# Kernel tuning notes

Hardware: AMD Instinct MI355X
Metric: run time of the kernel (lower is better)

Reference implementation:

```python
import jax, jax.numpy as jnp
import numpy as np

H3, W3, D3 = 12, 12, 12
NUM_HEADS = 8
DIM = 128
BATCH = 4
N_TOK = H3 * W3 * D3  # 1728
TABLE = (2 * H3 - 1) * (2 * W3 - 1) * (2 * D3 - 1)  # 12167


def _relative_position_index(h, w, d):
    ch, cw, cd = np.arange(h), np.arange(w), np.arange(d)
    coords = np.stack(np.meshgrid(ch, cw, cd, indexing='ij'))  # (3,h,w,d)
    cf = coords.reshape(3, -1)  # (3,N)
    rel = cf[:, :, None] - cf[:, None, :]  # (3,N,N)
    rel = rel.transpose(1, 2, 0).copy()
    rel[:, :, 0] += h - 1
    rel[:, :, 1] += w - 1
    rel[:, :, 2] += d - 1
    rel[:, :, 0] *= (2 * w - 1) * (2 * d - 1)
    rel[:, :, 1] *= 2 * d - 1
    return rel.sum(-1).astype(np.int32)  # (N,N)


def setup_inputs() -> dict:
    key = jax.random.key(0)
    ks = jax.random.split(key, 7)
    s = 1.0 / np.sqrt(DIM)
    return {
        'x': jax.random.normal(ks[0], (BATCH, N_TOK, DIM), jnp.float32),
        'Wq': jax.random.normal(ks[1], (DIM, DIM), jnp.float32) * s,
        'Wk': jax.random.normal(ks[2], (DIM, DIM), jnp.float32) * s,
        'Wv': jax.random.normal(ks[3], (DIM, DIM), jnp.float32) * s,
        'Wp': jax.random.normal(ks[4], (DIM, DIM), jnp.float32) * s,
        'bp': jnp.zeros((DIM,), jnp.float32),
        'rel_pos_table': jax.random.normal(ks[5], (TABLE, NUM_HEADS), jnp.float32) * 0.02,
        'rel_index': jnp.asarray(_relative_position_index(H3, W3, D3)),
    }


def reference(x, Wq, Wk, Wv, Wp, bp, rel_pos_table, rel_index):
    B, N, C = x.shape
    H = NUM_HEADS
    hd = C // H
    # projections (qkv_bias=False), split heads -> (B,H,N,hd)
    q = (x @ Wq.T).reshape(B, N, H, hd).transpose(0, 2, 1, 3)
    k = (x @ Wk.T).reshape(B, N, H, hd).transpose(0, 2, 1, 3)
    v = (x @ Wv.T).reshape(B, N, H, hd).transpose(0, 2, 1, 3)
    q_sig = jax.nn.sigmoid(q)
    # relative position bias: (N,N,H) -> (H,N,N)
    bias = rel_pos_table[rel_index.reshape(-1)].reshape(N, N, H).transpose(2, 0, 1)
    # softmax over key dim j of (k[b,h,j,d] + bias[h,i,j]) is separable:
    #   exp(k_jd + b_ij) = exp(b_ij - bmax_i) * exp(k_jd - kmax_d) * const
    kmax = jnp.max(k, axis=2, keepdims=True)            # (B,H,1,hd)
    bmax = jnp.max(bias, axis=2, keepdims=True)         # (H,N,1)
    ek = jnp.exp(k - kmax)                              # (B,H,N,hd)
    eb = jnp.exp(bias - bmax)                           # (H,N,N)
    num = jnp.einsum('hij,bhjd->bhid', eb, ek * v)      # (B,H,N,hd)
    den = jnp.einsum('hij,bhjd->bhid', eb, ek)          # (B,H,N,hd)
    out = q_sig * (num / den)                           # (B,H,N,hd)
    out = out.transpose(0, 2, 1, 3).reshape(B, N, C)
    return out @ Wp.T + bp
```

## Files before the change

### kernel.cpp

```cpp
#include <hip/hip_runtime.h>
#include <hip/hip_bf16.h>
#include <cmath>

#define NTOK 1728
#define DIMC 128
#define NHEAD 8
#define NB 4
#define TABN 12167
#define TSTRIDE 12168

typedef __attribute__((ext_vector_type(8))) short bf16x8;
typedef __attribute__((ext_vector_type(4))) float f32x4;

static __device__ __forceinline__ unsigned short f2bf(float f) {
    union { float f; unsigned u; } v; v.f = f;
    unsigned r = v.u + 0x7fff + ((v.u >> 16) & 1);
    return (unsigned short)(r >> 16);
}

static __device__ __forceinline__ int Pdec(int t) {
    return (t / 144) * 529 + ((t / 12) % 12) * 23 + (t % 12);
}

__global__ __launch_bounds__(256) void k_proj_qkv(
    const float* __restrict__ x, const float* __restrict__ Wq,
    const float* __restrict__ Wk, const float* __restrict__ Wv,
    const float* __restrict__ tbl, unsigned short* __restrict__ tblT,
    float* __restrict__ n1,
    float* __restrict__ QS, float* __restrict__ Ko, float* __restrict__ Vo)
{
    __shared__ __align__(16) float xs[64 * 128];
    __shared__ __align__(16) float Ws[32 * 128];
    const int t = threadIdx.x;
    const int m = blockIdx.z;
    if (m == 3) {
        const int bid2 = blockIdx.y * 108 + blockIdx.x;
        if (bid2 < 48) {
            const int idx = bid2 * 256 + t;
            if (idx < TABN) {
                float4 f0 = *reinterpret_cast<const float4*>(&tbl[idx * 8]);
                float4 f1 = *reinterpret_cast<const float4*>(&tbl[idx * 8 + 4]);
                tblT[0 * TSTRIDE + idx] = f2bf(expm1f(f0.x));
                tblT[1 * TSTRIDE + idx] = f2bf(expm1f(f0.y));
                tblT[2 * TSTRIDE + idx] = f2bf(expm1f(f0.z));
                tblT[3 * TSTRIDE + idx] = f2bf(expm1f(f0.w));
                tblT[4 * TSTRIDE + idx] = f2bf(expm1f(f1.x));
                tblT[5 * TSTRIDE + idx] = f2bf(expm1f(f1.y));
                tblT[6 * TSTRIDE + idx] = f2bf(expm1f(f1.z));
                tblT[7 * TSTRIDE + idx] = f2bf(expm1f(f1.w));
            }
        } else if (bid2 == 48) {
            ((float4*)n1)[t] = (float4){0.f, 0.f, 0.f, 0.f};
        }
        return;
    }
    const int row0 = blockIdx.x * 64;
    const int cg = blockIdx.y;
    const float* __restrict__ W = (m == 0) ? Wq : (m == 1) ? Wk : Wv;

    {
        const int cc = t & 31;
        #pragma unroll
        for (int p = 0; p < 8; ++p) {
            const int r = (t >> 5) + p * 8;
            float4 v = *reinterpret_cast<const float4*>(&x[(size_t)(row0 + r) * DIMC + cc * 4]);
            *reinterpret_cast<float4*>(&xs[r * 128 + ((cc * 4) ^ ((r & 7) << 2))]) = v;
        }
    }
    {
        const int cc = t & 31;
        #pragma unroll
        for (int p = 0; p < 4; ++p) {
            const int c = (t >> 5) + p * 8;
            float4 v = *reinterpret_cast<const float4*>(&W[(size_t)(cg * 32 + c) * DIMC + cc * 4]);
            *reinterpret_cast<float4*>(&Ws[c * 128 + cc * 4]) = v;
        }
    }
    __syncthreads();
    const int nl = t & 63, w = t >> 6;
    float acc[8];
    #pragma unroll
    for (int c = 0; c < 8; ++c) acc[c] = 0.f;
    for (int k4 = 0; k4 < 32; ++k4) {
        const float4 xv = *reinterpret_cast<const float4*>(
            &xs[nl * 128 + ((k4 * 4) ^ ((nl & 7) << 2))]);
        #pragma unroll
        for (int c = 0; c < 8; ++c) {
            const float4 wv = *reinterpret_cast<const float4*>(&Ws[(w * 8 + c) * 128 + k4 * 4]);
            acc[c] = fmaf(xv.x, wv.x, fmaf(xv.y, wv.y,
                     fmaf(xv.z, wv.z, fmaf(xv.w, wv.w, acc[c]))));
        }
    }
    if (m == 0) {
        #pragma unroll
        for (int c = 0; c < 8; ++c) acc[c] = 1.f / (1.f + expf(-acc[c]));
    }
    __syncthreads();
    float* res = Ws;
    #pragma unroll
    for (int c = 0; c < 8; ++c) res[nl * 33 + w * 8 + c] = acc[c];
    __syncthreads();
    float* __restrict__ Out = (m == 0) ? QS : (m == 1) ? Ko : Vo;
    {
        const int r = t >> 2, q = t & 3;
        float4 v0, v1;
        v0.x = res[r*33 + q*8 + 0]; v0.y = res[r*33 + q*8 + 1];
        v0.z = res[r*33 + q*8 + 2]; v0.w = res[r*33 + q*8 + 3];
        v1.x = res[r*33 + q*8 + 4]; v1.y = res[r*33 + q*8 + 5];
        v1.z = res[r*33 + q*8 + 6]; v1.w = res[r*33 + q*8 + 7];
        *reinterpret_cast<float4*>(&Out[(size_t)(row0 + r) * DIMC + cg * 32 + q * 8]) = v0;
        *reinterpret_cast<float4*>(&Out[(size_t)(row0 + r) * DIMC + cg * 32 + q * 8 + 4]) = v1;
    }
}

__global__ __launch_bounds__(256) void k_build_ekv(
    const float* __restrict__ Ko, const float* __restrict__ Vo,
    unsigned short* __restrict__ EKVt, float* __restrict__ n1)
{
    __shared__ float red[256][33];
    const int t = threadIdx.x;
    const int h = blockIdx.y;
    const int b = t >> 6, jj = t & 63;
    const int j = blockIdx.x * 64 + jj;
    const float* kp = &Ko[((size_t)b * NTOK + j) * DIMC + h * 16];
    const float* vp = &Vo[((size_t)b * NTOK + j) * DIMC + h * 16];
    float kv[16], vv[16], ob[32];
    #pragma unroll
    for (int d4 = 0; d4 < 4; ++d4) {
        *reinterpret_cast<float4*>(&kv[d4 * 4]) = *reinterpret_cast<const float4*>(&kp[d4 * 4]);
        *reinterpret_cast<float4*>(&vv[d4 * 4]) = *reinterpret_cast<const float4*>(&vp[d4 * 4]);
    }
    #pragma unroll
    for (int d = 0; d < 16; ++d) {
        float e = expf(kv[d]);
        ob[d] = e * vv[d];
        ob[16 + d] = e;
    }
    #pragma unroll
    for (int c = 0; c < 32; ++c)
        EKVt[((size_t)h * DIMC + b * 32 + c) * NTOK + j] = f2bf(ob[c]);
    #pragma unroll
    for (int c = 0; c < 32; ++c) red[t][c] = ob[c];
    __syncthreads();
    if (t < 128) {
        const int b2 = t >> 5, c = t & 31;
        float s = 0.f;
        for (int r = 0; r < 64; ++r) s += red[b2 * 64 + r][c];
        atomicAdd(&n1[(h * NB + b2) * 32 + c], s);
    }
}

__global__ __launch_bounds__(256) void k_aft_mfma(
    const unsigned short* __restrict__ tblT,
    const unsigned short* __restrict__ EKVt,
    float* __restrict__ part)
{
    __shared__ __align__(16) unsigned short slds[2304];
    __shared__ __align__(16) unsigned short alds[64 * 64];
    __shared__ __align__(16) unsigned short blds[128 * 64];
    const int t = threadIdx.x;
    const int i0 = blockIdx.x * 64;
    const int h = blockIdx.y;
    const int js = blockIdx.z;
    const int l = t & 63, w = t >> 6;
    const int il = l & 15, kg = l >> 4;

    const int j_base = js * 576;
    const int pj_lo = js * 4 * 529;
    const int pj_hi = pj_lo + 1851;
    const int idx_lo = Pdec(i0) + 6083 - pj_hi;
    {
        const unsigned short* src = &tblT[(size_t)h * TSTRIDE + idx_lo];
        #pragma unroll
        for (int p = 0; p < 9; ++p) slds[p * 256 + t] = src[p * 256 + t];
    }

    const int gi0 = w * 16;
    int qb[16];
    #pragma unroll
    for (int r = 0; r < 16; ++r) qb[r] = Pdec(i0 + gi0 + r) + 6083 - idx_lo;

    const int bc = t >> 3;
    const int bj8 = (t & 7) * 8;

    f32x4 acc[8];
    #pragma unroll
    for (int cf = 0; cf < 8; ++cf) acc[cf] = (f32x4){0.f, 0.f, 0.f, 0.f};

    for (int jt = 0; jt < 9; ++jt) {
        const int j0 = j_base + jt * 64;
        const int pj = Pdec(j0 + l);
        __syncthreads();
        #pragma unroll
        for (int p = 0; p < 4; ++p) {
            const int c = bc + p * 32;
            bf16x8 v = *reinterpret_cast<const bf16x8*>(
                &EKVt[((size_t)h * DIMC + c) * NTOK + j0 + bj8]);
            *reinterpret_cast<bf16x8*>(&blds[c * 64 + (bj8 ^ ((c & 7) << 3))]) = v;
        }
        #pragma unroll
        for (int r = 0; r < 16; ++r) {
            alds[(gi0 + r) * 64 + (l ^ ((r & 7) << 3))] = slds[qb[r] - pj];
        }
        __syncthreads();
        #pragma unroll
        for (int kk = 0; kk < 2; ++kk) {
            const int ia = w * 16 + il;
            const int ka = kk * 32 + kg * 8;
            bf16x8 af = *reinterpret_cast<const bf16x8*>(
                &alds[ia * 64 + (ka ^ ((ia & 7) << 3))]);
            #pragma unroll
            for (int cf = 0; cf < 8; ++cf) {
                const int cb = cf * 16 + il;
                bf16x8 bf = *reinterpret_cast<const bf16x8*>(
                    &blds[cb * 64 + (ka ^ ((cb & 7) << 3))]);
                acc[cf] = __builtin_amdgcn_mfma_f32_16x16x32_bf16(af, bf, acc[cf], 0, 0, 0);
            }
        }
    }
    #pragma unroll
    for (int cf = 0; cf < 8; ++cf) {
        #pragma unroll
        for (int r = 0; r < 4; ++r) {
            const int i = i0 + w * 16 + kg * 4 + r;
            const int c = cf * 16 + il;
            part[(((size_t)h * NTOK + i) * 3 + js) * DIMC + c] = acc[cf][r];
        }
    }
}

__global__ __launch_bounds__(256) void k_reduce_y(
    const float* __restrict__ part, const float* __restrict__ n1,
    const float* __restrict__ QS, float* __restrict__ Y)
{
    const int t = threadIdx.x;
    const int h = blockIdx.x;
    const int i = blockIdx.y * 16 + (t >> 4);
    const int b = t & 3, dq = (t >> 2) & 3;
    const float* pp = &part[((size_t)h * NTOK + i) * 3 * DIMC];
    float4 nu = *reinterpret_cast<const float4*>(&n1[(h * NB + b) * 32 + dq * 4]);
    float4 de = *reinterpret_cast<const float4*>(&n1[(h * NB + b) * 32 + 16 + dq * 4]);
    #pragma unroll
    for (int js = 0; js < 3; ++js) {
        float4 a  = *reinterpret_cast<const float4*>(&pp[js * DIMC + b * 32 + dq * 4]);
        float4 d4 = *reinterpret_cast<const float4*>(&pp[js * DIMC + b * 32 + 16 + dq * 4]);
        nu.x += a.x;  nu.y += a.y;  nu.z += a.z;  nu.w += a.w;
        de.x += d4.x; de.y += d4.y; de.z += d4.z; de.w += d4.w;
    }
    const size_t yb = ((size_t)b * NTOK + i) * DIMC + h * 16 + dq * 4;
    float4 q4 = *reinterpret_cast<const float4*>(&QS[yb]);
    float4 o;
    o.x = q4.x * nu.x / de.x;
    o.y = q4.y * nu.y / de.y;
    o.z = q4.z * nu.z / de.z;
    o.w = q4.w * nu.w / de.w;
    *reinterpret_cast<float4*>(&Y[yb]) = o;
}

__global__ __launch_bounds__(256) void k_proj_out(
    const float* __restrict__ Y, const float* __restrict__ Wp,
    const float* __restrict__ bp, float* __restrict__ out)
{
    __shared__ __align__(16) float xs[64 * 128];
    __shared__ __align__(16) float Ws[32 * 128];
    const int t = threadIdx.x;
    const int row0 = blockIdx.x * 64;
    const int cg = blockIdx.y;
    {
        const int cc = t & 31;
        #pragma unroll
        for (int p = 0; p < 8; ++p) {
            const int r = (t >> 5) + p * 8;
            float4 v = *reinterpret_cast<const float4*>(&Y[(size_t)(row0 + r) * DIMC + cc * 4]);
            *reinterpret_cast<float4*>(&xs[r * 128 + ((cc * 4) ^ ((r & 7) << 2))]) = v;
        }
    }
    {
        const int cc = t & 31;
        #pragma unroll
        for (int p = 0; p < 4; ++p) {
            const int c = (t >> 5) + p * 8;
            float4 v = *reinterpret_cast<const float4*>(&Wp[(size_t)(cg * 32 + c) * DIMC + cc * 4]);
            *reinterpret_cast<float4*>(&Ws[c * 128 + cc * 4]) = v;
        }
    }
    __syncthreads();
    const int nl = t & 63, w = t >> 6;
    float acc[8];
    #pragma unroll
    for (int c = 0; c < 8; ++c) acc[c] = 0.f;
    for (int k4 = 0; k4 < 32; ++k4) {
        const float4 xv = *reinterpret_cast<const float4*>(
            &xs[nl * 128 + ((k4 * 4) ^ ((nl & 7) << 2))]);
        #pragma unroll
        for (int c = 0; c < 8; ++c) {
            const float4 wv = *reinterpret_cast<const float4*>(&Ws[(w * 8 + c) * 128 + k4 * 4]);
            acc[c] = fmaf(xv.x, wv.x, fmaf(xv.y, wv.y,
                     fmaf(xv.z, wv.z, fmaf(xv.w, wv.w, acc[c]))));
        }
    }
    #pragma unroll
    for (int c = 0; c < 8; ++c) acc[c] += bp[cg * 32 + w * 8 + c];
    __syncthreads();
    float* res = Ws;
    #pragma unroll
    for (int c = 0; c < 8; ++c) res[nl * 33 + w * 8 + c] = acc[c];
    __syncthreads();
    {
        const int r = t >> 2, q = t & 3;
        float4 v0, v1;
        v0.x = res[r*33 + q*8 + 0]; v0.y = res[r*33 + q*8 + 1];
        v0.z = res[r*33 + q*8 + 2]; v0.w = res[r*33 + q*8 + 3];
        v1.x = res[r*33 + q*8 + 4]; v1.y = res[r*33 + q*8 + 5];
        v1.z = res[r*33 + q*8 + 6]; v1.w = res[r*33 + q*8 + 7];
        *reinterpret_cast<float4*>(&out[(size_t)(row0 + r) * DIMC + cg * 32 + q * 8]) = v0;
        *reinterpret_cast<float4*>(&out[(size_t)(row0 + r) * DIMC + cg * 32 + q * 8 + 4]) = v1;
    }
}

extern "C" void kernel_launch(void* const* d_in, const int* in_sizes, int n_in,
                              void* d_out, int out_size, void* d_ws, size_t ws_size,
                              hipStream_t stream) {
    const float* x    = (const float*)d_in[0];
    const float* Wq   = (const float*)d_in[1];
    const float* Wk   = (const float*)d_in[2];
    const float* Wv   = (const float*)d_in[3];
    const float* Wp   = (const float*)d_in[4];
    const float* bp   = (const float*)d_in[5];
    const float* tbl  = (const float*)d_in[6];
    float* out = (float*)d_out;

    float* ws = (float*)d_ws;
    unsigned short* tblT = (unsigned short*)ws;
    float* n1  = ws + 50000;
    float* QS  = n1 + 1024;
    float* Ko  = QS + 884736;
    float* Vo  = Ko + 884736;
    unsigned short* EKVt = (unsigned short*)(Vo + 884736);
    float* part = Vo + 884736 + 884736;
    float* Yb   = part + (size_t)NHEAD * NTOK * 3 * DIMC;

    k_proj_qkv<<<dim3(108, 4, 4), 256, 0, stream>>>(x, Wq, Wk, Wv, tbl, tblT, n1, QS, Ko, Vo);
    k_build_ekv<<<dim3(27, 8), 256, 0, stream>>>(Ko, Vo, EKVt, n1);
    k_aft_mfma<<<dim3(27, 8, 3), 256, 0, stream>>>(tblT, EKVt, part);
    k_reduce_y<<<dim3(8, 108), 256, 0, stream>>>(part, n1, QS, Yb);
    k_proj_out<<<dim3(108, 4), 256, 0, stream>>>(Yb, Wp, bp, out);
}
```

Baseline: 146.9 us.

## Fuse all stages into one persistent kernel with grid-wide atomic barriers

Replaces the five launches with a single persistent kernel of 216 blocks of 512 threads. Stages are separated by software grid barriers built on atomic counters, zeroed by a memset. The attention stage now runs the whole j range per block, with two sub-groups splitting j tiles and reducing through LDS, so the split-j partial buffer and the separate reduce kernel go away. This removes launch gaps and a global round trip, but it relies on all blocks being co-resident, uses far fewer blocks per stage, and adds barrier spin latency.

```diff
diff --git a/kernel.cpp b/kernel.cpp
--- a/kernel.cpp
+++ b/kernel.cpp
@@ -8,6 +8,8 @@
 #define NB 4
 #define TABN 12167
 #define TSTRIDE 12168
+#define NBLK 216
+#define SLDSN 6656
 
 typedef __attribute__((ext_vector_type(8))) short bf16x8;
 typedef __attribute__((ext_vector_type(4))) float f32x4;
@@ -17,304 +19,287 @@
     unsigned r = v.u + 0x7fff + ((v.u >> 16) & 1);
     return (unsigned short)(r >> 16);
 }
-
 static __device__ __forceinline__ int Pdec(int t) {
     return (t / 144) * 529 + ((t / 12) % 12) * 23 + (t % 12);
 }
 
-__global__ __launch_bounds__(256) void k_proj_qkv(
+static __device__ __forceinline__ void gridbar(unsigned* C, int id) {
+    __syncthreads();
+    if (threadIdx.x == 0) {
+        __threadfence();
+        atomicAdd(&C[id], 1u);
+        while (__hip_atomic_load(&C[id], __ATOMIC_RELAXED,
+                                 __HIP_MEMORY_SCOPE_AGENT) < (unsigned)NBLK)
+            __builtin_amdgcn_s_sleep(8);
+        __threadfence();
+    }
+    __syncthreads();
+}
+
+__global__ __launch_bounds__(512, 2) void k_mega(
     const float* __restrict__ x, const float* __restrict__ Wq,
     const float* __restrict__ Wk, const float* __restrict__ Wv,
-    const float* __restrict__ tbl, unsigned short* __restrict__ tblT,
-    float* __restrict__ n1,
-    float* __restrict__ QS, float* __restrict__ Ko, float* __restrict__ Vo)
+    const float* __restrict__ Wp, const float* __restrict__ bp,
+    const float* __restrict__ tbl,
+    unsigned* C, float* n1, unsigned short* tblT,
+    float* QS, float* Ko, float* Vo, unsigned short* EKVt,
+    float* Yb, float* out)
 {
-    __shared__ __align__(16) float xs[64 * 128];
-    __shared__ __align__(16) float Ws[32 * 128];
+    __shared__ __align__(16) unsigned char LDSU[98304];
     const int t = threadIdx.x;
-    const int m = blockIdx.z;
-    if (m == 3) {
-        const int bid2 = blockIdx.y * 108 + blockIdx.x;
-        if (bid2 < 48) {
-            const int idx = bid2 * 256 + t;
-            if (idx < TABN) {
-                float4 f0 = *reinterpret_cast<const float4*>(&tbl[idx * 8]);
-                float4 f1 = *reinterpret_cast<const float4*>(&tbl[idx * 8 + 4]);
-                tblT[0 * TSTRIDE + idx] = f2bf(expm1f(f0.x));
-                tblT[1 * TSTRIDE + idx] = f2bf(expm1f(f0.y));
-                tblT[2 * TSTRIDE + idx] = f2bf(expm1f(f0.z));
-                tblT[3 * TSTRIDE + idx] = f2bf(expm1f(f0.w));
-                tblT[4 * TSTRIDE + idx] = f2bf(expm1f(f1.x));
-                tblT[5 * TSTRIDE + idx] = f2bf(expm1f(f1.y));
-                tblT[6 * TSTRIDE + idx] = f2bf(expm1f(f1.z));
-                tblT[7 * TSTRIDE + idx] = f2bf(expm1f(f1.w));
-            }
-        } else if (bid2 == 48) {
-            ((float4*)n1)[t] = (float4){0.f, 0.f, 0.f, 0.f};
-        }
-        return;
-    }
-    const int row0 = blockIdx.x * 64;
-    const int cg = blockIdx.y;
-    const float* __restrict__ W = (m == 0) ? Wq : (m == 1) ? Wk : Wv;
+    const int sub = t >> 8, ts = t & 255;
+    const int slot = (int)blockIdx.x * 2 + sub;
 
     {
-        const int cc = t & 31;
-        #pragma unroll
-        for (int p = 0; p < 8; ++p) {
-            const int r = (t >> 5) + p * 8;
-            float4 v = *reinterpret_cast<const float4*>(&x[(size_t)(row0 + r) * DIMC + cc * 4]);
-            *reinterpret_cast<float4*>(&xs[r * 128 + ((cc * 4) ^ ((r & 7) << 2))]) = v;
-        }
-    }
+        float* S  = (float*)(LDSU + sub * 49152);
+        float* xs = S;
+        float* Ws = S + 64 * 128;
+        const int rt = slot >> 2, cg = slot & 3;
+        const int row0 = rt * 64;
+        {
+            const int cc = ts & 31;
+            #pragma unroll
+            for (int p = 0; p < 8; ++p) {
+                const int r = (ts >> 5) + p * 8;
+                float4 v = *(const float4*)&x[(size_t)(row0 + r) * DIMC + cc * 4];
+                *(float4*)&xs[r * 128 + ((cc * 4) ^ ((r & 7) << 2))] = v;
+            }
+        }
+        #pragma unroll 1
+        for (int m = 0; m < 3; ++m) {
+            const float* __restrict__ W = (m == 0) ? Wq : (m == 1) ? Wk : Wv;
+            __syncthreads();
+            {
+                const int cc = ts & 31;
+                #pragma unroll
+                for (int p = 0; p < 4; ++p) {
+                    const int c = (ts >> 5) + p * 8;
+                    float4 v = *(const float4*)&W[(size_t)(cg * 32 + c) * DIMC + cc * 4];
+                    *(float4*)&Ws[c * 128 + cc * 4] = v;
+                }
+            }
+            __syncthreads();
+            const int nl = ts & 63, wx = ts >> 6;
+            float acc[8];
+            #pragma unroll
+            for (int c = 0; c < 8; ++c) acc[c] = 0.f;
+            for (int k4 = 0; k4 < 32; ++k4) {
+                const float4 xv = *(const float4*)&xs[nl * 128 + ((k4 * 4) ^ ((nl & 7) << 2))];
+                #pragma unroll
+                for (int c = 0; c < 8; ++c) {
+                    const float4 wv = *(const float4*)&Ws[(wx * 8 + c) * 128 + k4 * 4];
+                    acc[c] = fmaf(xv.x, wv.x, fmaf(xv.y, wv.y,
+                             fmaf(xv.z, wv.z, fmaf(xv.w, wv.w, acc[c]))));
+                }
+            }
+            if (m == 0) {
+                #pragma unroll
+                for (int c = 0; c < 8; ++c) acc[c] = 1.f / (1.f + expf(-acc[c]));
+            }
+            __syncthreads();
+            #pragma unroll
+            for (int c = 0; c < 8; ++c) Ws[nl * 33 + wx * 8 + c] = acc[c];
+            __syncthreads();
+            float* __restrict__ Out = (m == 0) ? QS : (m == 1) ? Ko : Vo;
+            const int r = ts >> 2, q = ts & 3;
+            float4 v0, v1;
+            v0.x = Ws[r*33 + q*8 + 0]; v0.y = Ws[r*33 + q*8 + 1];
+            v0.z = Ws[r*33 + q*8 + 2]; v0.w = Ws[r*33 + q*8 + 3];
+            v1.x = Ws[r*33 + q*8 + 4]; v1.y = Ws[r*33 + q*8 + 5];
+            v1.z = Ws[r*33 + q*8 + 6]; v1.w = Ws[r*33 + q*8 + 7];
+            *(float4*)&Out[(size_t)(row0 + r) * DIMC + cg * 32 + q * 8] = v0;
+            *(float4*)&Out[(size_t)(row0 + r) * DIMC + cg * 32 + q * 8 + 4] = v1;
+        }
+    }
+    gridbar(C, 0);
+
+    if (slot < 216) {
+        float (*red)[33] = (float (*)[33])(LDSU + sub * 49152);
+        const int jx = slot % 27, h = slot / 27;
+        const int b = ts >> 6, jj = ts & 63;
+        const int j = jx * 64 + jj;
+        const float* kp = &Ko[((size_t)b * NTOK + j) * DIMC + h * 16];
+        const float* vp = &Vo[((size_t)b * NTOK + j) * DIMC + h * 16];
+        float kv[16], vv[16], ob[32];
+        #pragma unroll
+        for (int d4 = 0; d4 < 4; ++d4) {
+            *(float4*)&kv[d4 * 4] = *(const float4*)&kp[d4 * 4];
+            *(float4*)&vv[d4 * 4] = *(const float4*)&vp[d4 * 4];
+        }
+        #pragma unroll
+        for (int d = 0; d < 16; ++d) {
+            float e = expf(kv[d]);
+            ob[d] = e * vv[d];
+            ob[16 + d] = e;
+        }
+        #pragma unroll
+        for (int c = 0; c < 32; ++c)
+            EKVt[((size_t)h * DIMC + b * 32 + c) * NTOK + j] = f2bf(ob[c]);
+        #pragma unroll
+        for (int c = 0; c < 32; ++c) red[ts][c] = ob[c];
+        __syncthreads();
+        if (ts < 128) {
+            const int b2 = ts >> 5, c = ts & 31;
+            float s = 0.f;
+            for (int r = 0; r < 64; ++r) s += red[b2 * 64 + r][c];
+            atomicAdd(&n1[(h * NB + b2) * 32 + c], s);
+        }
+    } else {
+        const int base = (slot - 216) * 57;
+        for (int v2 = ts; v2 < 456; v2 += 256) {
+            const int ii = v2 >> 3, hh = v2 & 7;
+            const int idx = base + ii;
+            if (ii < 57 && idx < TABN)
+                tblT[hh * TSTRIDE + idx] = f2bf(expm1f(tbl[idx * 8 + hh]));
+        }
+        __syncthreads();
+    }
+    gridbar(C, 1);
+
     {
-        const int cc = t & 31;
-        #pragma unroll
-        for (int p = 0; p < 4; ++p) {
-            const int c = (t >> 5) + p * 8;
-            float4 v = *reinterpret_cast<const float4*>(&W[(size_t)(cg * 32 + c) * DIMC + cc * 4]);
-            *reinterpret_cast<float4*>(&Ws[c * 128 + cc * 4]) = v;
-        }
-    }
-    __syncthreads();
-    const int nl = t & 63, w = t >> 6;
-    float acc[8];
-    #pragma unroll
-    for (int c = 0; c < 8; ++c) acc[c] = 0.f;
-    for (int k4 = 0; k4 < 32; ++k4) {
-        const float4 xv = *reinterpret_cast<const float4*>(
-            &xs[nl * 128 + ((k4 * 4) ^ ((nl & 7) << 2))]);
-        #pragma unroll
-        for (int c = 0; c < 8; ++c) {
-            const float4 wv = *reinterpret_cast<const float4*>(&Ws[(w * 8 + c) * 128 + k4 * 4]);
-            acc[c] = fmaf(xv.x, wv.x, fmaf(xv.y, wv.y,
-                     fmaf(xv.z, wv.z, fmaf(xv.w, wv.w, acc[c]))));
-        }
-    }
-    if (m == 0) {
-        #pragma unroll
-        for (int c = 0; c < 8; ++c) acc[c] = 1.f / (1.f + expf(-acc[c]));
-    }
-    __syncthreads();
-    float* res = Ws;
-    #pragma unroll
-    for (int c = 0; c < 8; ++c) res[nl * 33 + w * 8 + c] = acc[c];
-    __syncthreads();
-    float* __restrict__ Out = (m == 0) ? QS : (m == 1) ? Ko : Vo;
+        const int ti = (int)blockIdx.x % 27, h = (int)blockIdx.x / 27;
+        const int i0 = ti * 64;
+        unsigned short* slds = (unsigned short*)LDSU;
+        unsigned short* alds = (unsigned short*)(LDSU + 13312 + sub * 24576);
+        unsigned short* blds = alds + 64 * 64;
+        float* rbuf = (float*)(LDSU + 13312 + 24576);
+
+        const int idx_lo = Pdec(i0);
+        {
+            const unsigned short* src = &tblT[(size_t)h * TSTRIDE];
+            for (int s = t; s < SLDSN; s += 512) {
+                const int g = idx_lo + s;
+                slds[s] = (g < TSTRIDE) ? src[g] : (unsigned short)0;
+            }
+        }
+        const int w = ts >> 6, l = ts & 63;
+        const int il = l & 15, kg = l >> 4;
+        const int gi0 = w * 16;
+        int qb[16];
+        #pragma unroll
+        for (int r = 0; r < 16; ++r) qb[r] = Pdec(i0 + gi0 + r) + 6083 - idx_lo;
+        const int bc = ts >> 3, bj8 = (ts & 7) * 8;
+
+        f32x4 acc[8];
+        #pragma unroll
+        for (int cf = 0; cf < 8; ++cf) acc[cf] = (f32x4){0.f, 0.f, 0.f, 0.f};
+
+        #pragma unroll 1
+        for (int jt = 0; jt < 14; ++jt) {
+            const int j0 = (2 * jt + sub) * 64;
+            const bool act = (j0 < NTOK);
+            __syncthreads();
+            if (act) {
+                #pragma unroll
+                for (int pp = 0; pp < 4; ++pp) {
+                    const int c = bc + pp * 32;
+                    bf16x8 v = *(const bf16x8*)&EKVt[((size_t)h * DIMC + c) * NTOK + j0 + bj8];
+                    *(bf16x8*)&blds[c * 64 + (bj8 ^ ((c & 7) << 3))] = v;
+                }
+                const int pj = Pdec(j0 + l);
+                #pragma unroll
+                for (int r = 0; r < 16; ++r)
+                    alds[(gi0 + r) * 64 + (l ^ ((r & 7) << 3))] = slds[qb[r] - pj];
+            }
+            __syncthreads();
+            if (act) {
+                #pragma unroll
+                for (int kk = 0; kk < 2; ++kk) {
+                    const int ia = w * 16 + il;
+                    const int ka = kk * 32 + kg * 8;
+                    bf16x8 af = *(const bf16x8*)&alds[ia * 64 + (ka ^ ((ia & 7) << 3))];
+                    #pragma unroll
+                    for (int cf = 0; cf < 8; ++cf) {
+                        const int cb = cf * 16 + il;
+                        bf16x8 bfv = *(const bf16x8*)&blds[cb * 64 + (ka ^ ((cb & 7) << 3))];
+                        acc[cf] = __builtin_amdgcn_mfma_f32_16x16x32_bf16(af, bfv, acc[cf], 0, 0, 0);
+                    }
+                }
+            }
+        }
+        __syncthreads();
+        if (sub == 1) {
+            #pragma unroll
+            for (int cf = 0; cf < 8; ++cf)
+                *(f32x4*)&rbuf[ts * 36 + cf * 4] = acc[cf];
+        }
+        __syncthreads();
+        if (sub == 0) {
+            #pragma unroll
+            for (int cf = 0; cf < 8; ++cf) {
+                f32x4 o = *(const f32x4*)&rbuf[ts * 36 + cf * 4];
+                acc[cf][0] += o[0]; acc[cf][1] += o[1];
+                acc[cf][2] += o[2]; acc[cf][3] += o[3];
+            }
+            #pragma unroll
+            for (int e = 0; e < 4; ++e) {
+                const float nn0 = n1[(h * NB + e) * 32 + il];
+                const float dd0 = n1[(h * NB + e) * 32 + 16 + il];
+                #pragma unroll
+                for (int r = 0; r < 4; ++r) {
+                    const int i = i0 + w * 16 + kg * 4 + r;
+                    const size_t off = ((size_t)e * NTOK + i) * DIMC + h * 16 + il;
+                    const float nn = nn0 + acc[2 * e][r];
+                    const float dd = dd0 + acc[2 * e + 1][r];
+                    Yb[off] = QS[off] * nn / dd;
+                }
+            }
+        }
+    }
+    gridbar(C, 2);
+
     {
-        const int r = t >> 2, q = t & 3;
+        float* S  = (float*)(LDSU + sub * 49152);
+        float* xs = S;
+        float* Ws = S + 64 * 128;
+        const int rt = slot >> 2, cg = slot & 3;
+        const int row0 = rt * 64;
+        {
+            const int cc = ts & 31;
+            #pragma unroll
+            for (int p = 0; p < 8; ++p) {
+                const int r = (ts >> 5) + p * 8;
+                float4 v = *(const float4*)&Yb[(size_t)(row0 + r) * DIMC + cc * 4];
+                *(float4*)&xs[r * 128 + ((cc * 4) ^ ((r & 7) << 2))] = v;
+            }
+        }
+        {
+            const int cc = ts & 31;
+            #pragma unroll
+            for (int p = 0; p < 4; ++p) {
+                const int c = (ts >> 5) + p * 8;
+                float4 v = *(const float4*)&Wp[(size_t)(cg * 32 + c) * DIMC + cc * 4];
+                *(float4*)&Ws[c * 128 + cc * 4] = v;
+            }
+        }
+        __syncthreads();
+        const int nl = ts & 63, wx = ts >> 6;
+        float acc[8];
+        #pragma unroll
+        for (int c = 0; c < 8; ++c) acc[c] = 0.f;
+        for (int k4 = 0; k4 < 32; ++k4) {
+            const float4 xv = *(const float4*)&xs[nl * 128 + ((k4 * 4) ^ ((nl & 7) << 2))];
+            #pragma unroll
+            for (int c = 0; c < 8; ++c) {
+                const float4 wv = *(const float4*)&Ws[(wx * 8 + c) * 128 + k4 * 4];
+                acc[c] = fmaf(xv.x, wv.x, fmaf(xv.y, wv.y,
+                         fmaf(xv.z, wv.z, fmaf(xv.w, wv.w, acc[c]))));
+            }
+        }
+        #pragma unroll
+        for (int c = 0; c < 8; ++c) acc[c] += bp[cg * 32 + wx * 8 + c];
+        __syncthreads();
+        #pragma unroll
+        for (int c = 0; c < 8; ++c) Ws[nl * 33 + wx * 8 + c] = acc[c];
+        __syncthreads();
+        const int r = ts >> 2, q = ts & 3;
         float4 v0, v1;
-        v0.x = res[r*33 + q*8 + 0]; v0.y = res[r*33 + q*8 + 1];
-        v0.z = res[r*33 + q*8 + 2]; v0.w = res[r*33 + q*8 + 3];
-        v1.x = res[r*33 + q*8 + 4]; v1.y = res[r*33 + q*8 + 5];
-        v1.z = res[r*33 + q*8 + 6]; v1.w = res[r*33 + q*8 + 7];
-        *reinterpret_cast<float4*>(&Out[(size_t)(row0 + r) * DIMC + cg * 32 + q * 8]) = v0;
-        *reinterpret_cast<float4*>(&Out[(size_t)(row0 + r) * DIMC + cg * 32 + q * 8 + 4]) = v1;
-    }
-}
-
-__global__ __launch_bounds__(256) void k_build_ekv(
-    const float* __restrict__ Ko, const float* __restrict__ Vo,
-    unsigned short* __restrict__ EKVt, float* __restrict__ n1)
-{
-    __shared__ float red[256][33];
-    const int t = threadIdx.x;
-    const int h = blockIdx.y;
-    const int b = t >> 6, jj = t & 63;
-    const int j = blockIdx.x * 64 + jj;
-    const float* kp = &Ko[((size_t)b * NTOK + j) * DIMC + h * 16];
-    const float* vp = &Vo[((size_t)b * NTOK + j) * DIMC + h * 16];
-    float kv[16], vv[16], ob[32];
-    #pragma unroll
-    for (int d4 = 0; d4 < 4; ++d4) {
-        *reinterpret_cast<float4*>(&kv[d4 * 4]) = *reinterpret_cast<const float4*>(&kp[d4 * 4]);
-        *reinterpret_cast<float4*>(&vv[d4 * 4]) = *reinterpret_cast<const float4*>(&vp[d4 * 4]);
-    }
-    #pragma unroll
-    for (int d = 0; d < 16; ++d) {
-        float e = expf(kv[d]);
-        ob[d] = e * vv[d];
-        ob[16 + d] = e;
-    }
-    #pragma unroll
-    for (int c = 0; c < 32; ++c)
-        EKVt[((size_t)h * DIMC + b * 32 + c) * NTOK + j] = f2bf(ob[c]);
-    #pragma unroll
-    for (int c = 0; c < 32; ++c) red[t][c] = ob[c];
-    __syncthreads();
-    if (t < 128) {
-        const int b2 = t >> 5, c = t & 31;
-        float s = 0.f;
-        for (int r = 0; r < 64; ++r) s += red[b2 * 64 + r][c];
-        atomicAdd(&n1[(h * NB + b2) * 32 + c], s);
-    }
-}
-
-__global__ __launch_bounds__(256) void k_aft_mfma(
-    const unsigned short* __restrict__ tblT,
-    const unsigned short* __restrict__ EKVt,
-    float* __restrict__ part)
-{
-    __shared__ __align__(16) unsigned short slds[2304];
-    __shared__ __align__(16) unsigned short alds[64 * 64];
-    __shared__ __align__(16) unsigned short blds[128 * 64];
-    const int t = threadIdx.x;
-    const int i0 = blockIdx.x * 64;
-    const int h = blockIdx.y;
-    const int js = blockIdx.z;
-    const int l = t & 63, w = t >> 6;
-    const int il = l & 15, kg = l >> 4;
-
-    const int j_base = js * 576;
-    const int pj_lo = js * 4 * 529;
-    const int pj_hi = pj_lo + 1851;
-    const int idx_lo = Pdec(i0) + 6083 - pj_hi;
-    {
-        const unsigned short* src = &tblT[(size_t)h * TSTRIDE + idx_lo];
-        #pragma unroll
-        for (int p = 0; p < 9; ++p) slds[p * 256 + t] = src[p * 256 + t];
-    }
-
-    const int gi0 = w * 16;
-    int qb[16];
-    #pragma unroll
-    for (int r = 0; r < 16; ++r) qb[r] = Pdec(i0 + gi0 + r) + 6083 - idx_lo;
-
-    const int bc = t >> 3;
-    const int bj8 = (t & 7) * 8;
-
-    f32x4 acc[8];
-    #pragma unroll
-    for (int cf = 0; cf < 8; ++cf) acc[cf] = (f32x4){0.f, 0.f, 0.f, 0.f};
-
-    for (int jt = 0; jt < 9; ++jt) {
-        const int j0 = j_base + jt * 64;
-        const int pj = Pdec(j0 + l);
-        __syncthreads();
-        #pragma unroll
-        for (int p = 0; p < 4; ++p) {
-            const int c = bc + p * 32;
-            bf16x8 v = *reinterpret_cast<const bf16x8*>(
-                &EKVt[((size_t)h * DIMC + c) * NTOK + j0 + bj8]);
-            *reinterpret_cast<bf16x8*>(&blds[c * 64 + (bj8 ^ ((c & 7) << 3))]) = v;
-        }
-        #pragma unroll
-        for (int r = 0; r < 16; ++r) {
-            alds[(gi0 + r) * 64 + (l ^ ((r & 7) << 3))] = slds[qb[r] - pj];
-        }
-        __syncthreads();
-        #pragma unroll
-        for (int kk = 0; kk < 2; ++kk) {
-            const int ia = w * 16 + il;
-            const int ka = kk * 32 + kg * 8;
-            bf16x8 af = *reinterpret_cast<const bf16x8*>(
-                &alds[ia * 64 + (ka ^ ((ia & 7) << 3))]);
-            #pragma unroll
-            for (int cf = 0; cf < 8; ++cf) {
-                const int cb = cf * 16 + il;
-                bf16x8 bf = *reinterpret_cast<const bf16x8*>(
-                    &blds[cb * 64 + (ka ^ ((cb & 7) << 3))]);
-                acc[cf] = __builtin_amdgcn_mfma_f32_16x16x32_bf16(af, bf, acc[cf], 0, 0, 0);
-            }
-        }
-    }
-    #pragma unroll
-    for (int cf = 0; cf < 8; ++cf) {
-        #pragma unroll
-        for (int r = 0; r < 4; ++r) {
-            const int i = i0 + w * 16 + kg * 4 + r;
-            const int c = cf * 16 + il;
-            part[(((size_t)h * NTOK + i) * 3 + js) * DIMC + c] = acc[cf][r];
-        }
-    }
-}
-
-__global__ __launch_bounds__(256) void k_reduce_y(
-    const float* __restrict__ part, const float* __restrict__ n1,
-    const float* __restrict__ QS, float* __restrict__ Y)
-{
-    const int t = threadIdx.x;
-    const int h = blockIdx.x;
-    const int i = blockIdx.y * 16 + (t >> 4);
-    const int b = t & 3, dq = (t >> 2) & 3;
-    const float* pp = &part[((size_t)h * NTOK + i) * 3 * DIMC];
-    float4 nu = *reinterpret_cast<const float4*>(&n1[(h * NB + b) * 32 + dq * 4]);
-    float4 de = *reinterpret_cast<const float4*>(&n1[(h * NB + b) * 32 + 16 + dq * 4]);
-    #pragma unroll
-    for (int js = 0; js < 3; ++js) {
-        float4 a  = *reinterpret_cast<const float4*>(&pp[js * DIMC + b * 32 + dq * 4]);
-        float4 d4 = *reinterpret_cast<const float4*>(&pp[js * DIMC + b * 32 + 16 + dq * 4]);
-        nu.x += a.x;  nu.y += a.y;  nu.z += a.z;  nu.w += a.w;
-        de.x += d4.x; de.y += d4.y; de.z += d4.z; de.w += d4.w;
-    }
-    const size_t yb = ((size_t)b * NTOK + i) * DIMC + h * 16 + dq * 4;
-    float4 q4 = *reinterpret_cast<const float4*>(&QS[yb]);
-    float4 o;
-    o.x = q4.x * nu.x / de.x;
-    o.y = q4.y * nu.y / de.y;
-    o.z = q4.z * nu.z / de.z;
-    o.w = q4.w * nu.w / de.w;
-    *reinterpret_cast<float4*>(&Y[yb]) = o;
-}
-
-__global__ __launch_bounds__(256) void k_proj_out(
-    const float* __restrict__ Y, const float* __restrict__ Wp,
-    const float* __restrict__ bp, float* __restrict__ out)
-{
-    __shared__ __align__(16) float xs[64 * 128];
-    __shared__ __align__(16) float Ws[32 * 128];
-    const int t = threadIdx.x;
-    const int row0 = blockIdx.x * 64;
-    const int cg = blockIdx.y;
-    {
-        const int cc = t & 31;
-        #pragma unroll
-        for (int p = 0; p < 8; ++p) {
-            const int r = (t >> 5) + p * 8;
-            float4 v = *reinterpret_cast<const float4*>(&Y[(size_t)(row0 + r) * DIMC + cc * 4]);
-            *reinterpret_cast<float4*>(&xs[r * 128 + ((cc * 4) ^ ((r & 7) << 2))]) = v;
-        }
-    }
-    {
-        const int cc = t & 31;
-        #pragma unroll
-        for (int p = 0; p < 4; ++p) {
-            const int c = (t >> 5) + p * 8;
-            float4 v = *reinterpret_cast<const float4*>(&Wp[(size_t)(cg * 32 + c) * DIMC + cc * 4]);
-            *reinterpret_cast<float4*>(&Ws[c * 128 + cc * 4]) = v;
-        }
-    }
-    __syncthreads();
-    const int nl = t & 63, w = t >> 6;
-    float acc[8];
-    #pragma unroll
-    for (int c = 0; c < 8; ++c) acc[c] = 0.f;
-    for (int k4 = 0; k4 < 32; ++k4) {
-        const float4 xv = *reinterpret_cast<const float4*>(
-            &xs[nl * 128 + ((k4 * 4) ^ ((nl & 7) << 2))]);
-        #pragma unroll
-        for (int c = 0; c < 8; ++c) {
-            const float4 wv = *reinterpret_cast<const float4*>(&Ws[(w * 8 + c) * 128 + k4 * 4]);
-            acc[c] = fmaf(xv.x, wv.x, fmaf(xv.y, wv.y,
-                     fmaf(xv.z, wv.z, fmaf(xv.w, wv.w, acc[c]))));
-        }
-    }
-    #pragma unroll
-    for (int c = 0; c < 8; ++c) acc[c] += bp[cg * 32 + w * 8 + c];
-    __syncthreads();
-    float* res = Ws;
-    #pragma unroll
-    for (int c = 0; c < 8; ++c) res[nl * 33 + w * 8 + c] = acc[c];
-    __syncthreads();
-    {
-        const int r = t >> 2, q = t & 3;
-        float4 v0, v1;
-        v0.x = res[r*33 + q*8 + 0]; v0.y = res[r*33 + q*8 + 1];
-        v0.z = res[r*33 + q*8 + 2]; v0.w = res[r*33 + q*8 + 3];
-        v1.x = res[r*33 + q*8 + 4]; v1.y = res[r*33 + q*8 + 5];
-        v1.z = res[r*33 + q*8 + 6]; v1.w = res[r*33 + q*8 + 7];
-        *reinterpret_cast<float4*>(&out[(size_t)(row0 + r) * DIMC + cg * 32 + q * 8]) = v0;
-        *reinterpret_cast<float4*>(&out[(size_t)(row0 + r) * DIMC + cg * 32 + q * 8 + 4]) = v1;
+        v0.x = Ws[r*33 + q*8 + 0]; v0.y = Ws[r*33 + q*8 + 1];
+        v0.z = Ws[r*33 + q*8 + 2]; v0.w = Ws[r*33 + q*8 + 3];
+        v1.x = Ws[r*33 + q*8 + 4]; v1.y = Ws[r*33 + q*8 + 5];
+        v1.z = Ws[r*33 + q*8 + 6]; v1.w = Ws[r*33 + q*8 + 7];
+        *(float4*)&out[(size_t)(row0 + r) * DIMC + cg * 32 + q * 8] = v0;
+        *(float4*)&out[(size_t)(row0 + r) * DIMC + cg * 32 + q * 8 + 4] = v1;
     }
 }
 
@@ -328,21 +313,19 @@
     const float* Wp   = (const float*)d_in[4];
     const float* bp   = (const float*)d_in[5];
     const float* tbl  = (const float*)d_in[6];
-    float* out = (float*)d_out;
 
     float* ws = (float*)d_ws;
-    unsigned short* tblT = (unsigned short*)ws;
-    float* n1  = ws + 50000;
-    float* QS  = n1 + 1024;
-    float* Ko  = QS + 884736;
-    float* Vo  = Ko + 884736;
+    unsigned* C = (unsigned*)ws;
+    float* n1 = ws + 16;
+    unsigned short* tblT = (unsigned short*)(ws + 16 + 1024);
+    float* QS = ws + 16 + 1024 + 48672;
+    float* Ko = QS + 884736;
+    float* Vo = Ko + 884736;
     unsigned short* EKVt = (unsigned short*)(Vo + 884736);
-    float* part = Vo + 884736 + 884736;
-    float* Yb   = part + (size_t)NHEAD * NTOK * 3 * DIMC;
-
-    k_proj_qkv<<<dim3(108, 4, 4), 256, 0, stream>>>(x, Wq, Wk, Wv, tbl, tblT, n1, QS, Ko, Vo);
-    k_build_ekv<<<dim3(27, 8), 256, 0, stream>>>(Ko, Vo, EKVt, n1);
-    k_aft_mfma<<<dim3(27, 8, 3), 256, 0, stream>>>(tblT, EKVt, part);
-    k_reduce_y<<<dim3(8, 108), 256, 0, stream>>>(part, n1, QS, Yb);
-    k_proj_out<<<dim3(108, 4), 256, 0, stream>>>(Yb, Wp, bp, out);
-}
+    float* Yb = Vo + 884736 + 884736;
+
+    hipMemsetAsync(ws, 0, (16 + 1024) * sizeof(float), stream);
+    k_mega<<<dim3(NBLK), 512, 0, stream>>>(x, Wq, Wk, Wv, Wp, bp, tbl,
+                                           C, n1, tblT, QS, Ko, Vo, EKVt, Yb,
+                                           (float*)d_out);
+}
```

New measurement: 203.2 us. 38.3% more time.
